# Kernel tuning notes

Measured on AMD Instinct MI355X. Metric: run time of the kernel, lower is better.

The kernel has to match this reference:

```python
import jax, jax.numpy as jnp
import numpy as np

B, T, D, H, A = 1024, 128, 64, 256, 8  # batch, seq_len, state_dim, hidden_dim, action_dim


def setup_inputs() -> dict:
    key = jax.random.key(0)
    ks = jax.random.split(key, 12)
    k = 1.0 / np.sqrt(H)  # PyTorch LSTM/Linear default init range
    u = lambda kk, shape: jax.random.uniform(kk, shape, jnp.float32, -k, k)
    return {
        "state": jax.random.normal(ks[0], (B, 1, D), jnp.float32),
        "gamma": jnp.ones((D,), jnp.float32),
        "beta": jnp.zeros((D,), jnp.float32),
        "W_ih0": u(ks[1], (4 * H, D)),
        "W_hh0": u(ks[2], (4 * H, H)),
        "b_ih0": u(ks[3], (4 * H,)),
        "b_hh0": u(ks[4], (4 * H,)),
        "W_ih1": u(ks[5], (4 * H, H)),
        "W_hh1": u(ks[6], (4 * H, H)),
        "b_ih1": u(ks[7], (4 * H,)),
        "b_hh1": u(ks[8], (4 * H,)),
        "fcW": u(ks[9], (A, H)),
        "fcb": u(ks[10], (A,)),
        "seq_len": T,
    }


def _lstm_cell(x, h, c, Wih, Whh, b):
    # PyTorch gate order: input, forget, cell(g), output
    g = x @ Wih.T + h @ Whh.T + b
    i, f, gg, o = jnp.split(g, 4, axis=-1)
    c_new = jax.nn.sigmoid(f) * c + jax.nn.sigmoid(i) * jnp.tanh(gg)
    h_new = jax.nn.sigmoid(o) * jnp.tanh(c_new)
    return h_new, c_new


def reference(state, gamma, beta, W_ih0, W_hh0, b_ih0, b_hh0,
              W_ih1, W_hh1, b_ih1, b_hh1, fcW, fcb, seq_len):
    # state: [B, 1, D]; the same (layernormed) input is fed every timestep,
    # only the LSTM hidden/cell state evolves.
    x = state[:, 0, :]  # [B, D]
    mu = x.mean(-1, keepdims=True)
    var = ((x - mu) ** 2).mean(-1, keepdims=True)
    xn = (x - mu) * jax.lax.rsqrt(var + 1e-5) * gamma + beta  # LayerNorm(state_dim)

    b0 = b_ih0 + b_hh0
    b1 = b_ih1 + b_hh1
    bsz = x.shape[0]
    hdim = W_hh0.shape[1]
    z = jnp.zeros((bsz, hdim), x.dtype)
    init = (z, z, z, z)  # (h0, c0, h1, c1); h=None -> zeros in torch

    def step(carry, _):
        h0, c0, h1, c1 = carry
        h0, c0 = _lstm_cell(xn, h0, c0, W_ih0, W_hh0, b0)  # layer 0
        h1, c1 = _lstm_cell(h0, h1, c1, W_ih1, W_hh1, b1)  # layer 1
        action = jnp.tanh(h1 @ fcW.T + fcb)  # [B, A]
        return (h0, c0, h1, c1), action

    _, actions = jax.lax.scan(step, init, None, length=seq_len)  # [T, B, A]
    return jnp.transpose(actions, (1, 0, 2))  # [B, T, A]
```

## Files before the change

### kernel.cpp

```cpp
#include <hip/hip_runtime.h>
#include <math.h>

#define B_    1024
#define T_    128
#define D_    64
#define H_    256
#define A_    8

#define NB    32
#define SL    8
#define FSTR  16

typedef __attribute__((ext_vector_type(8))) short short8;
typedef __attribute__((ext_vector_type(4))) float floatx4;

__device__ __forceinline__ short f2bf(float f) {
    union { float f; unsigned u; } x; x.f = f;
    return (short)((x.u + 0x7FFFu + ((x.u >> 16) & 1u)) >> 16);
}
__device__ __forceinline__ float bf2f(short s) {
    union { unsigned u; float f; } x;
    x.u = ((unsigned)(unsigned short)s) << 16;
    return x.f;
}
__device__ __forceinline__ float sigm(float x) {
    return __builtin_amdgcn_rcpf(1.0f + __expf(-x));
}
__device__ __forceinline__ float ftanh(float x) {
    float t = __expf(-2.0f * fabsf(x));
    float r = (1.0f - t) * __builtin_amdgcn_rcpf(1.0f + t);
    return copysignf(r, x);
}

__device__ __forceinline__ void cell_update(floatx4 aA, floatx4 aB, float* cpair,
                                            short* __restrict__ Hw, size_t rowbase,
                                            int colbase, int hi, int rsel) {
    floatx4 tA, tB;
#pragma unroll
    for (int r = 0; r < 4; ++r) {
        tA[r] = __shfl_xor(aA[r], 8, 64);
        tB[r] = __shfl_xor(aB[r], 8, 64);
    }
#pragma unroll
    for (int rr = 0; rr < 2; ++rr) {
        int r = rsel + rr;
        float gi = hi ? tA[r] : aA[r];
        float gf = hi ? aA[r] : tA[r];
        float gg = hi ? tB[r] : aB[r];
        float go = hi ? aB[r] : tB[r];
        float cn = sigm(gf) * cpair[rr] + sigm(gi) * ftanh(gg);
        float hn = sigm(go) * ftanh(cn);
        cpair[rr] = cn;
        Hw[(rowbase + r) * H_ + colbase] = f2bf(hn);
    }
}

template<int UH>
__global__ void __launch_bounds__(256)
actor_kernel(const float* __restrict__ state, const float* __restrict__ gamma,
             const float* __restrict__ beta,  const float* __restrict__ Wih0,
             const float* __restrict__ Whh0,  const float* __restrict__ bih0,
             const float* __restrict__ bhh0,  const float* __restrict__ Wih1,
             const float* __restrict__ Whh1,  const float* __restrict__ bih1,
             const float* __restrict__ bhh1,  const float* __restrict__ fcW,
             const float* __restrict__ fcb,   float* __restrict__ out,
             unsigned* __restrict__ flags, unsigned* __restrict__ aux,
             short* __restrict__ Hb0, short* __restrict__ Hb1)
{
    constexpr int NGROUPS = 16 / UH;
    constexpr int M       = 64 * UH;
    constexpr int FCR     = 2 * UH;

    __shared__ __attribute__((aligned(16))) short sWp[16384];

    const int blk  = blockIdx.x;
    const int tid  = threadIdx.x;
    const int lane = tid & 63;
    const int wave = tid >> 6;

    int* sMapi = (int*)sWp;
    if (tid == 0) {
        unsigned xcc;
        asm volatile("s_getreg_b32 %0, hwreg(HW_REG_XCC_ID)" : "=s"(xcc));
        xcc &= 7u;
        unsigned r = atomicAdd(&aux[xcc * 16], 1u);
        __hip_atomic_fetch_add(&aux[256], 1u, __ATOMIC_ACQ_REL,
                               __HIP_MEMORY_SCOPE_AGENT);
        while (__hip_atomic_load(&aux[256], __ATOMIC_RELAXED,
                                 __HIP_MEMORY_SCOPE_AGENT) < (unsigned)gridDim.x)
            __builtin_amdgcn_s_sleep(1);
        __builtin_amdgcn_fence(__ATOMIC_ACQUIRE, "agent");
        int pre = 0, tot = 0; bool ok = true;
        for (int x = 0; x < 8; ++x) {
            int cx = (int)__hip_atomic_load(&aux[x * 16], __ATOMIC_RELAXED,
                                            __HIP_MEMORY_SCOPE_AGENT);
            if (cx & 31) ok = false;
            if (x < (int)xcc) pre += cx >> 5;
            tot += cx >> 5;
        }
        if (tot != NGROUPS) ok = false;
        sMapi[0] = ok ? (pre + (int)(r >> 5)) : (blk % NGROUPS);
        sMapi[1] = ok ? (int)(r & 31)         : (blk / NGROUPS);
        sMapi[2] = ok ? 1 : 0;
    }
    __syncthreads();
    const int  g     = sMapi[0];
    const int  s     = sMapi[1];
    const bool fastp = (sMapi[2] != 0);
    __syncthreads();
    const int gM = g * M;

    const int q4   = lane >> 4;
    const int l15  = lane & 15;
    const int jj   = l15 & 7;
    const int hi   = l15 >> 3;
    const int rg0  = hi * H_ + s * SL + jj;
    const int rg1  = (2 + hi) * H_ + s * SL + jj;
    const int mrow = wave * 16 + q4 * 4;
    const int colbase = s * SL + jj;
    const int rsel = hi * 2;

    const float b0v0 = bih0[rg0] + bhh0[rg0];
    const float b0v1 = bih0[rg1] + bhh0[rg1];
    const float b1v0 = bih1[rg0] + bhh1[rg0];
    const float b1v1 = bih1[rg1] + bhh1[rg1];

    floatx4 pre0a[UH], pre0b[UH];
    float* sXn = (float*)sWp;
    {
        const float* w0 = Wih0 + (size_t)rg0 * D_;
        const float* w1 = Wih0 + (size_t)rg1 * D_;
        for (int u = 0; u < UH; ++u) {
            if (tid < 64) {
                const float* xr = state + (size_t)(gM + u * 64 + tid) * D_;
                float mu = 0.f;
                for (int d = 0; d < D_; ++d) mu += xr[d];
                mu *= (1.0f / D_);
                float var = 0.f;
                for (int d = 0; d < D_; ++d) { float t = xr[d] - mu; var += t * t; }
                var *= (1.0f / D_);
                float is = rsqrtf(var + 1e-5f);
                for (int d = 0; d < D_; ++d)
                    sXn[tid * 65 + d] = (xr[d] - mu) * is * gamma[d] + beta[d];
            }
            __syncthreads();
#pragma unroll
            for (int r = 0; r < 4; ++r) { pre0a[u][r] = b0v0; pre0b[u][r] = b0v1; }
            for (int d = 0; d < D_; ++d) {
                float wa = w0[d], wb = w1[d];
#pragma unroll
                for (int r = 0; r < 4; ++r) {
                    float xv = sXn[(mrow + r) * 65 + d];
                    pre0a[u][r] += xv * wa;
                    pre0b[u][r] += xv * wb;
                }
            }
            __syncthreads();
        }
    }

    const int fo = lane >> 3, fk8 = lane & 7;
    float fcw_r[32];
#pragma unroll
    for (int kk = 0; kk < 32; ++kk) fcw_r[kk] = fcW[fo * H_ + fk8 * 32 + kk];
    const float fcb_r = fcb[fo];

    short8 bw0[16];
    {
        const float* wA = Whh0 + (size_t)rg0 * H_ + q4 * 8;
        const float* wB = Whh0 + (size_t)rg1 * H_ + q4 * 8;
#pragma unroll
        for (int kt = 0; kt < 8; ++kt) {
            short8 sa, sb;
#pragma unroll
            for (int j = 0; j < 8; ++j) {
                sa[j] = f2bf(wA[kt * 32 + j]);
                sb[j] = f2bf(wB[kt * 32 + j]);
            }
            bw0[2 * kt]     = sa;
            bw0[2 * kt + 1] = sb;
        }
    }

    for (int idx = tid; idx < 16384; idx += 256) {
        int kt = idx >> 11, rem = idx & 2047;
        int c = rem >> 9, rem2 = rem & 511;
        int ln = rem2 >> 3, j = rem2 & 7;
        int q4_ = ln >> 4, l15_ = ln & 15;
        int n = (c & 1) * 16 + l15_;
        int r = (n >> 3) * H_ + s * SL + (n & 7);
        int k = kt * 32 + q4_ * 8 + j;
        float v = (c >> 1) ? Whh1[(size_t)r * H_ + k] : Wih1[(size_t)r * H_ + k];
        sWp[idx] = f2bf(v);
    }
    float c0[UH][2], c1[UH][2];
    for (int u = 0; u < UH; ++u) { c0[u][0]=c0[u][1]=0.f; c1[u][0]=c1[u][1]=0.f; }
    __syncthreads();

    const short* ldsB1 = sWp + lane * 8;

    const int BH = B_ * H_;
    for (int ph = 0; ph <= T_ + 1; ++ph) {
        const short* H0r  = Hb0 + ((ph + 1) & 1) * BH;
        short*       H0w  = Hb0 + (ph & 1) * BH;
        const short* H1r2 = Hb1 + (ph & 1) * BH;
        short*       H1w  = Hb1 + ((ph + 1) & 1) * BH;

        const bool doL0 = (ph < T_);
        const bool doL1 = (ph >= 1 && ph <= T_);

        if (ph >= 2 && wave < FCR) {
            int t = ph - 2;
            int b = FCR * s + wave;
            const short8* hp = (const short8*)(H1r2 + (size_t)(gM + b) * H_ + fk8 * 32);
            float sum = 0.f;
#pragma unroll
            for (int c8 = 0; c8 < 4; ++c8) {
                short8 hv = hp[c8];
#pragma unroll
                for (int j = 0; j < 8; ++j)
                    sum += bf2f(hv[j]) * fcw_r[c8 * 8 + j];
            }
            sum += __shfl_down(sum, 4, 8);
            sum += __shfl_down(sum, 2, 8);
            sum += __shfl_down(sum, 1, 8);
            if (fk8 == 0)
                out[((size_t)(gM + b) * T_ + t) * A_ + fo] = ftanh(sum + fcb_r);
        }

        if (doL0 || doL1) {
            for (int u = 0; u < UH; ++u) {
                short8 a0[8], a1[8];
                const size_t arow = (size_t)(gM + u * 64 + wave * 16 + l15) * H_ + q4 * 8;
                const short* ap = H0r + arow;
#pragma unroll
                for (int kt = 0; kt < 8; ++kt)
                    a0[kt] = *(const short8*)(ap + kt * 32);
                if (doL1) {
                    const short* cp = H1r2 + arow;
#pragma unroll
                    for (int kt = 0; kt < 8; ++kt)
                        a1[kt] = *(const short8*)(cp + kt * 32);
                }

                floatx4 l0a = pre0a[u], l0b = pre0b[u], l1a, l1b;
#pragma unroll
                for (int r = 0; r < 4; ++r) { l1a[r] = b1v0; l1b[r] = b1v1; }

#pragma unroll
                for (int kt = 0; kt < 8; ++kt) {
                    if (doL0) {
                        l0a = __builtin_amdgcn_mfma_f32_16x16x32_bf16(a0[kt], bw0[2*kt],   l0a, 0, 0, 0);
                        l0b = __builtin_amdgcn_mfma_f32_16x16x32_bf16(a0[kt], bw0[2*kt+1], l0b, 0, 0, 0);
                    }
                    if (doL1) {
                        short8 bia = *(const short8*)(ldsB1 + kt * 2048);
                        short8 bib = *(const short8*)(ldsB1 + kt * 2048 + 512);
                        short8 bha = *(const short8*)(ldsB1 + kt * 2048 + 1024);
                        short8 bhb = *(const short8*)(ldsB1 + kt * 2048 + 1536);
                        l1a = __builtin_amdgcn_mfma_f32_16x16x32_bf16(a0[kt], bia, l1a, 0, 0, 0);
                        l1b = __builtin_amdgcn_mfma_f32_16x16x32_bf16(a0[kt], bib, l1b, 0, 0, 0);
                        l1a = __builtin_amdgcn_mfma_f32_16x16x32_bf16(a1[kt], bha, l1a, 0, 0, 0);
                        l1b = __builtin_amdgcn_mfma_f32_16x16x32_bf16(a1[kt], bhb, l1b, 0, 0, 0);
                    }
                }

                size_t rowbase = (size_t)(gM + u * 64 + mrow);
                if (doL0) cell_update(l0a, l0b, c0[u], H0w, rowbase, colbase, hi, rsel);
                if (doL1) cell_update(l1a, l1b, c1[u], H1w, rowbase, colbase, hi, rsel);
            }
        }

        if (ph <= T_) {
            __syncthreads();
            const unsigned val = (unsigned)(ph + 2);
            if (tid == 0) {
                if (!fastp) __builtin_amdgcn_fence(__ATOMIC_RELEASE, "agent");
                __hip_atomic_store(&flags[(g * NB + s) * FSTR], val,
                                   __ATOMIC_RELAXED, __HIP_MEMORY_SCOPE_AGENT);
            }
            if (wave == 3 && lane < NB) {
                while (__hip_atomic_load(&flags[(g * NB + lane) * FSTR],
                                         __ATOMIC_RELAXED, __HIP_MEMORY_SCOPE_AGENT)
                       < val)
                    __builtin_amdgcn_s_sleep(1);
            }
            __syncthreads();
            if (fastp) { asm volatile("buffer_inv sc0" ::: "memory"); }
            else       { __builtin_amdgcn_fence(__ATOMIC_ACQUIRE, "agent"); }
        }
    }
}

extern "C" void kernel_launch(void* const* d_in, const int* in_sizes, int n_in,
                              void* d_out, int out_size, void* d_ws, size_t ws_size,
                              hipStream_t stream)
{
    const float* state = (const float*)d_in[0];
    const float* gamma = (const float*)d_in[1];
    const float* beta  = (const float*)d_in[2];
    const float* Wih0  = (const float*)d_in[3];
    const float* Whh0  = (const float*)d_in[4];
    const float* bih0  = (const float*)d_in[5];
    const float* bhh0  = (const float*)d_in[6];
    const float* Wih1  = (const float*)d_in[7];
    const float* Whh1  = (const float*)d_in[8];
    const float* bih1  = (const float*)d_in[9];
    const float* bhh1  = (const float*)d_in[10];
    const float* fcW   = (const float*)d_in[11];
    const float* fcb   = (const float*)d_in[12];
    float* out = (float*)d_out;

    unsigned* flags = (unsigned*)d_ws;
    unsigned* aux   = (unsigned*)((char*)d_ws + 32768);
    short* Hb0 = (short*)((char*)d_ws + 36864);
    short* Hb1 = Hb0 + 2 * B_ * H_;

    size_t zbytes = 36864 + (size_t)4 * B_ * H_ * sizeof(short);
    hipMemsetAsync(d_ws, 0, zbytes, stream);

    void* args[] = { &state, &gamma, &beta, &Wih0, &Whh0, &bih0, &bhh0,
                     &Wih1, &Whh1, &bih1, &bhh1, &fcW, &fcb, &out,
                     &flags, &aux, &Hb0, &Hb1 };

    int nb = 0;
    hipError_t qe = hipOccupancyMaxActiveBlocksPerMultiprocessor(
        &nb, (const void*)(actor_kernel<1>), 256, 0);
    if (qe != hipSuccess) { (void)hipGetLastError(); nb = 0; }

    if (nb >= 2) {
        hipError_t err = hipLaunchCooperativeKernel((const void*)(actor_kernel<1>),
                                                    dim3(512), dim3(256),
                                                    args, 0, stream);
        if (err != hipSuccess) {
            (void)hipGetLastError();
            actor_kernel<1><<<dim3(512), dim3(256), 0, stream>>>(
                state, gamma, beta, Wih0, Whh0, bih0, bhh0,
                Wih1, Whh1, bih1, bhh1, fcW, fcb, out, flags, aux, Hb0, Hb1);
        }
    } else {
        hipError_t err = hipLaunchCooperativeKernel((const void*)(actor_kernel<2>),
                                                    dim3(256), dim3(256),
                                                    args, 0, stream);
        if (err != hipSuccess) {
            (void)hipGetLastError();
            actor_kernel<2><<<dim3(256), dim3(256), 0, stream>>>(
                state, gamma, beta, Wih0, Whh0, bih0, bhh0,
                Wih1, Whh1, bih1, bhh1, fcW, fcb, out, flags, aux, Hb0, Hb1);
        }
    }
    (void)in_sizes; (void)n_in; (void)out_size; (void)ws_size;
}
```

Baseline: 1.133 ms.

## Hold layer-1 recurrent weights in registers and halve LDS footprint

Moves the W_hh1 bf16 fragments from shared memory into per-thread registers (bw1) alongside W_hh0, halving the LDS weight buffer to hold only W_ih1. The fc weights are no longer cached in registers and are re-read from global memory each step. The layernorm scratch is transposed to a d-major layout, and the launch bounds request two blocks per CU. The aim is to cut LDS traffic in the layer-1 MFMA loop, at the cost of heavy register pressure and possible spills, plus extra global reads in the fc head.

```diff
diff --git a/kernel.cpp b/kernel.cpp
--- a/kernel.cpp
+++ b/kernel.cpp
@@ -56,7 +56,7 @@
 }
 
 template<int UH>
-__global__ void __launch_bounds__(256)
+__global__ void __launch_bounds__(256, 2)
 actor_kernel(const float* __restrict__ state, const float* __restrict__ gamma,
              const float* __restrict__ beta,  const float* __restrict__ Wih0,
              const float* __restrict__ Whh0,  const float* __restrict__ bih0,
@@ -71,7 +71,7 @@
     constexpr int M       = 64 * UH;
     constexpr int FCR     = 2 * UH;
 
-    __shared__ __attribute__((aligned(16))) short sWp[16384];
+    __shared__ __attribute__((aligned(16))) short sWp[8192];
 
     const int blk  = blockIdx.x;
     const int tid  = threadIdx.x;
@@ -141,7 +141,7 @@
                 var *= (1.0f / D_);
                 float is = rsqrtf(var + 1e-5f);
                 for (int d = 0; d < D_; ++d)
-                    sXn[tid * 65 + d] = (xr[d] - mu) * is * gamma[d] + beta[d];
+                    sXn[d * 64 + tid] = (xr[d] - mu) * is * gamma[d] + beta[d];
             }
             __syncthreads();
 #pragma unroll
@@ -150,7 +150,7 @@
                 float wa = w0[d], wb = w1[d];
 #pragma unroll
                 for (int r = 0; r < 4; ++r) {
-                    float xv = sXn[(mrow + r) * 65 + d];
+                    float xv = sXn[d * 64 + mrow + r];
                     pre0a[u][r] += xv * wa;
                     pre0b[u][r] += xv * wb;
                 }
@@ -159,45 +159,45 @@
         }
     }
 
-    const int fo = lane >> 3, fk8 = lane & 7;
-    float fcw_r[32];
-#pragma unroll
-    for (int kk = 0; kk < 32; ++kk) fcw_r[kk] = fcW[fo * H_ + fk8 * 32 + kk];
-    const float fcb_r = fcb[fo];
-
-    short8 bw0[16];
+    short8 bw0[16], bw1[16];
     {
-        const float* wA = Whh0 + (size_t)rg0 * H_ + q4 * 8;
-        const float* wB = Whh0 + (size_t)rg1 * H_ + q4 * 8;
+        const float* a0p = Whh0 + (size_t)rg0 * H_ + q4 * 8;
+        const float* b0p = Whh0 + (size_t)rg1 * H_ + q4 * 8;
+        const float* a1p = Whh1 + (size_t)rg0 * H_ + q4 * 8;
+        const float* b1p = Whh1 + (size_t)rg1 * H_ + q4 * 8;
 #pragma unroll
         for (int kt = 0; kt < 8; ++kt) {
-            short8 sa, sb;
+            short8 sa, sb, sc, sd;
 #pragma unroll
             for (int j = 0; j < 8; ++j) {
-                sa[j] = f2bf(wA[kt * 32 + j]);
-                sb[j] = f2bf(wB[kt * 32 + j]);
-            }
-            bw0[2 * kt]     = sa;
-            bw0[2 * kt + 1] = sb;
-        }
-    }
-
-    for (int idx = tid; idx < 16384; idx += 256) {
-        int kt = idx >> 11, rem = idx & 2047;
+                sa[j] = f2bf(a0p[kt * 32 + j]);
+                sb[j] = f2bf(b0p[kt * 32 + j]);
+                sc[j] = f2bf(a1p[kt * 32 + j]);
+                sd[j] = f2bf(b1p[kt * 32 + j]);
+            }
+            bw0[2 * kt] = sa;  bw0[2 * kt + 1] = sb;
+            bw1[2 * kt] = sc;  bw1[2 * kt + 1] = sd;
+        }
+    }
+
+    for (int idx = tid; idx < 8192; idx += 256) {
+        int kt = idx >> 10, rem = idx & 1023;
         int c = rem >> 9, rem2 = rem & 511;
         int ln = rem2 >> 3, j = rem2 & 7;
         int q4_ = ln >> 4, l15_ = ln & 15;
-        int n = (c & 1) * 16 + l15_;
+        int n = c * 16 + l15_;
         int r = (n >> 3) * H_ + s * SL + (n & 7);
         int k = kt * 32 + q4_ * 8 + j;
-        float v = (c >> 1) ? Whh1[(size_t)r * H_ + k] : Wih1[(size_t)r * H_ + k];
-        sWp[idx] = f2bf(v);
+        sWp[idx] = f2bf(Wih1[(size_t)r * H_ + k]);
     }
     float c0[UH][2], c1[UH][2];
     for (int u = 0; u < UH; ++u) { c0[u][0]=c0[u][1]=0.f; c1[u][0]=c1[u][1]=0.f; }
     __syncthreads();
 
     const short* ldsB1 = sWp + lane * 8;
+    const int fo = lane >> 3, fk8 = lane & 7;
+    const float* fcwp = fcW + fo * H_ + fk8 * 32;
+    const float fcb_r = fcb[fo];
 
     const int BH = B_ * H_;
     for (int ph = 0; ph <= T_ + 1; ++ph) {
@@ -219,7 +219,7 @@
                 short8 hv = hp[c8];
 #pragma unroll
                 for (int j = 0; j < 8; ++j)
-                    sum += bf2f(hv[j]) * fcw_r[c8 * 8 + j];
+                    sum += bf2f(hv[j]) * fcwp[c8 * 8 + j];
             }
             sum += __shfl_down(sum, 4, 8);
             sum += __shfl_down(sum, 2, 8);
@@ -254,14 +254,12 @@
                         l0b = __builtin_amdgcn_mfma_f32_16x16x32_bf16(a0[kt], bw0[2*kt+1], l0b, 0, 0, 0);
                     }
                     if (doL1) {
-                        short8 bia = *(const short8*)(ldsB1 + kt * 2048);
-                        short8 bib = *(const short8*)(ldsB1 + kt * 2048 + 512);
-                        short8 bha = *(const short8*)(ldsB1 + kt * 2048 + 1024);
-                        short8 bhb = *(const short8*)(ldsB1 + kt * 2048 + 1536);
+                        short8 bia = *(const short8*)(ldsB1 + kt * 1024);
+                        short8 bib = *(const short8*)(ldsB1 + kt * 1024 + 512);
                         l1a = __builtin_amdgcn_mfma_f32_16x16x32_bf16(a0[kt], bia, l1a, 0, 0, 0);
                         l1b = __builtin_amdgcn_mfma_f32_16x16x32_bf16(a0[kt], bib, l1b, 0, 0, 0);
-                        l1a = __builtin_amdgcn_mfma_f32_16x16x32_bf16(a1[kt], bha, l1a, 0, 0, 0);
-                        l1b = __builtin_amdgcn_mfma_f32_16x16x32_bf16(a1[kt], bhb, l1b, 0, 0, 0);
+                        l1a = __builtin_amdgcn_mfma_f32_16x16x32_bf16(a1[kt], bw1[2*kt],   l1a, 0, 0, 0);
+                        l1b = __builtin_amdgcn_mfma_f32_16x16x32_bf16(a1[kt], bw1[2*kt+1], l1b, 0, 0, 0);
                     }
                 }
 
```

Measured after the change: 1.604 ms. +41.6%, slower.
